# Optimization experiments

Measured on AMD Instinct MI355X. Metric: run time of the kernel, lower is better.

The kernel has to match this reference:

```python
import jax, jax.numpy as jnp
import numpy as np

NUM_HEADS = 16
DIM_MODEL = 1024
DIM_K = DIM_MODEL // NUM_HEADS
B, S = 2, 2048


def _linear_params(key, d_in, d_out):
    kw, kb = jax.random.split(key)
    bound = 1.0 / np.sqrt(d_in)
    W = jax.random.uniform(kw, (d_out, d_in), jnp.float32, -bound, bound)
    b = jax.random.uniform(kb, (d_out,), jnp.float32, -bound, bound)
    return W, b


def setup_inputs() -> dict:
    key = jax.random.key(0)
    ks = jax.random.split(key, 7)
    Q_in = jax.random.normal(ks[0], (B, S, DIM_MODEL), jnp.float32)
    K_in = jax.random.normal(ks[1], (B, S, DIM_MODEL), jnp.float32)
    V_in = jax.random.normal(ks[2], (B, S, DIM_MODEL), jnp.float32)
    Wq, bq = _linear_params(ks[3], DIM_MODEL, DIM_MODEL)
    Wk, bk = _linear_params(ks[4], DIM_MODEL, DIM_MODEL)
    Wv, bv = _linear_params(ks[5], DIM_MODEL, DIM_MODEL)
    Wo, bo = _linear_params(ks[6], DIM_MODEL, DIM_MODEL)
    return {"Q_in": Q_in, "K_in": K_in, "V_in": V_in,
            "Wq": Wq, "bq": bq, "Wk": Wk, "bk": bk,
            "Wv": Wv, "bv": bv, "Wo": Wo, "bo": bo}


def reference(Q_in, K_in, V_in, Wq, bq, Wk, bk, Wv, bv, Wo, bo):
    # QKV projections (nn.Linear: x @ W.T + b)
    Q = Q_in @ Wq.T + bq
    K = K_in @ Wk.T + bk
    V = V_in @ Wv.T + bv
    # [B, S, D] -> [B, H, S, dk]
    def split_heads(x):
        return x.reshape(B, S, NUM_HEADS, DIM_K).transpose(0, 2, 1, 3)
    Qh, Kh, Vh = split_heads(Q), split_heads(K), split_heads(V)
    # Scaled dot-product attention
    scale = 1.0 / np.sqrt(DIM_K)
    scores = jnp.einsum('bhqd,bhkd->bhqk', Qh, Kh) * scale  # [B,H,S,S]
    attn = jax.nn.softmax(scores, axis=-1)
    out = jnp.einsum('bhqk,bhkd->bhqd', attn, Vh)  # [B,H,S,dk]
    # Merge heads -> [B, S, D]
    out = out.transpose(0, 2, 1, 3).reshape(B, S, DIM_MODEL)
    return out @ Wo.T + bo
```

## Files before the change

### kernel.cpp

```cpp
#include <hip/hip_runtime.h>
#include <stdint.h>

#define BB 2
#define SS 2048
#define DD 1024
#define HH 16
#define DKK 64
#define MT (BB*SS)

#define GSTRIDE 40
#define ASTRIDE 72

using short8  = __attribute__((ext_vector_type(8))) short;
using floatx4 = __attribute__((ext_vector_type(4))) float;
using u16x4   = __attribute__((ext_vector_type(4))) unsigned short;
typedef unsigned short u16;

__device__ __forceinline__ u16 f2b(float f) {
  union { float f; unsigned u; } v; v.f = f;
  return (u16)((v.u + 0x7FFFu + ((v.u >> 16) & 1u)) >> 16);
}
__device__ __forceinline__ void pack16(const float4* p, short8& lo, short8& hi) {
  float4 x0 = p[0], x1 = p[1], x2 = p[2], x3 = p[3];
  lo[0]=(short)f2b(x0.x); lo[1]=(short)f2b(x0.y); lo[2]=(short)f2b(x0.z); lo[3]=(short)f2b(x0.w);
  lo[4]=(short)f2b(x1.x); lo[5]=(short)f2b(x1.y); lo[6]=(short)f2b(x1.z); lo[7]=(short)f2b(x1.w);
  hi[0]=(short)f2b(x2.x); hi[1]=(short)f2b(x2.y); hi[2]=(short)f2b(x2.z); hi[3]=(short)f2b(x2.w);
  hi[4]=(short)f2b(x3.x); hi[5]=(short)f2b(x3.y); hi[6]=(short)f2b(x3.z); hi[7]=(short)f2b(x3.w);
}
__device__ __forceinline__ void gload16(const u16* g, u16* l) {
  __builtin_amdgcn_global_load_lds(
      (const __attribute__((address_space(1))) void*)g,
      (__attribute__((address_space(3))) void*)l, 16, 0, 0);
}

__global__ __launch_bounds__(256) void cast_all(
    const float* __restrict__ Qin, const float* __restrict__ Kin,
    const float* __restrict__ Vin, const float* __restrict__ Wq,
    const float* __restrict__ Wk,  const float* __restrict__ Wv,
    const float* __restrict__ Wo,
    u16* __restrict__ cQ, u16* __restrict__ cK, u16* __restrict__ cV,
    u16* __restrict__ cWq, u16* __restrict__ cWk, u16* __restrict__ cWv,
    u16* __restrict__ cWo)
{
  const int y = blockIdx.y;
  if (y >= 3 && blockIdx.x >= (DD*DD/8/256)) return;
  const float* s; u16* d;
  switch (y) {
    case 0: s = Qin; d = cQ;  break;
    case 1: s = Kin; d = cK;  break;
    case 2: s = Vin; d = cV;  break;
    case 3: s = Wq;  d = cWq; break;
    case 4: s = Wk;  d = cWk; break;
    case 5: s = Wv;  d = cWv; break;
    default: s = Wo; d = cWo; break;
  }
  const size_t g = (size_t)blockIdx.x * 256 + threadIdx.x;
  float4 x0 = ((const float4*)s)[g*2], x1 = ((const float4*)s)[g*2+1];
  short8 lo;
  lo[0]=(short)f2b(x0.x); lo[1]=(short)f2b(x0.y); lo[2]=(short)f2b(x0.z); lo[3]=(short)f2b(x0.w);
  lo[4]=(short)f2b(x1.x); lo[5]=(short)f2b(x1.y); lo[6]=(short)f2b(x1.z); lo[7]=(short)f2b(x1.w);
  ((short8*)d)[g] = lo;
}
__global__ __launch_bounds__(256) void cast_w3(
    const float* __restrict__ w0, const float* __restrict__ w1,
    const float* __restrict__ w2, u16* __restrict__ o)
{
  const float* s = (blockIdx.y == 0) ? w0 : (blockIdx.y == 1) ? w1 : w2;
  u16* d = o + (size_t)blockIdx.y * (DD * DD);
  const size_t g = (size_t)blockIdx.x * 256 + threadIdx.x;
  float4 x0 = ((const float4*)s)[g*2], x1 = ((const float4*)s)[g*2+1];
  short8 lo;
  lo[0]=(short)f2b(x0.x); lo[1]=(short)f2b(x0.y); lo[2]=(short)f2b(x0.z); lo[3]=(short)f2b(x0.w);
  lo[4]=(short)f2b(x1.x); lo[5]=(short)f2b(x1.y); lo[6]=(short)f2b(x1.z); lo[7]=(short)f2b(x1.w);
  ((short8*)d)[g] = lo;
}

template<bool OUT_F32>
__device__ __forceinline__ void gemm_async(
    const u16* __restrict__ A, const u16* __restrict__ W,
    const float* __restrict__ bias, void* __restrict__ Cv,
    const int K, const int N, const int m0, const int n0, const float scale)
{
  __shared__ __align__(16) u16 sA[128*64];
  __shared__ __align__(16) u16 sB[128*64];

  const int tid  = threadIdx.x;
  const int wave = tid >> 6;
  const int lane = tid & 63;
  const int quad = lane >> 4;
  const int lr   = lane & 15;
  const int wm   = wave >> 1;
  const int wn   = wave & 1;
  const int srow = lane >> 3;
  const int swz  = (((lane & 7) ^ ((srow & 1) << 2)) << 3);

  floatx4 acc[4][4];
#pragma unroll
  for (int i = 0; i < 4; ++i)
#pragma unroll
    for (int j = 0; j < 4; ++j) acc[i][j] = (floatx4){0.f, 0.f, 0.f, 0.f};

  const u16* pA[4]; const u16* pW[4];
#pragma unroll
  for (int c = 0; c < 4; ++c) {
    const int row = (wave + c*4) * 8 + srow;
    pA[c] = A + (size_t)(m0 + row) * K + swz;
    pW[c] = W + (size_t)(n0 + row) * K + swz;
  }

  const int nk = K >> 6;
  for (int kt = 0; kt < nk; ++kt) {
    const int k0 = kt << 6;
#pragma unroll
    for (int c = 0; c < 4; ++c) {
      gload16(pA[c] + k0, sA + (wave + c*4) * 512);
      gload16(pW[c] + k0, sB + (wave + c*4) * 512);
    }
    __syncthreads();

#pragma unroll
    for (int h2 = 0; h2 < 2; ++h2) {
      const int csel = (quad << 3) + ((h2 ^ (lr & 1)) << 5);
      short8 af[4], bf[4];
#pragma unroll
      for (int t = 0; t < 4; ++t) {
        af[t] = *(const short8*)(sA + (wm*64 + t*16 + lr)*64 + csel);
        bf[t] = *(const short8*)(sB + (wn*64 + t*16 + lr)*64 + csel);
      }
#pragma unroll
      for (int i = 0; i < 4; ++i)
#pragma unroll
        for (int j = 0; j < 4; ++j)
          acc[i][j] = __builtin_amdgcn_mfma_f32_16x16x32_bf16(af[i], bf[j], acc[i][j], 0, 0, 0);
    }
    __syncthreads();
  }

#pragma unroll
  for (int i = 0; i < 4; ++i) {
    const int mb = m0 + wm*64 + i*16 + quad*4;
#pragma unroll
    for (int j = 0; j < 4; ++j) {
      const int n = n0 + wn*64 + j*16 + lr;
      const float bsv = bias[n];
#pragma unroll
      for (int r = 0; r < 4; ++r) {
        const size_t idx = (size_t)(mb + r) * N + n;
        const float v = (acc[i][j][r] + bsv) * scale;
        if (OUT_F32) ((float*)Cv)[idx] = v;
        else         ((u16*)Cv)[idx]   = f2b(v);
      }
    }
  }
}

__global__ __launch_bounds__(256, 3) void gemm_qkv_async(
    const u16* __restrict__ cQ, const u16* __restrict__ cK, const u16* __restrict__ cV,
    const u16* __restrict__ cWq, const u16* __restrict__ cWk, const u16* __restrict__ cWv,
    const float* __restrict__ bq, const float* __restrict__ bk, const float* __restrict__ bv,
    u16* __restrict__ oQ, u16* __restrict__ oK, u16* __restrict__ oV)
{
  const int wsel = blockIdx.x >> 3;
  const int n0 = (blockIdx.x & 7) * 128;
  const int m0 = blockIdx.y * 128;
  const u16* A; const u16* W; const float* bias; u16* C;
  if (wsel == 0)      { A = cQ; W = cWq; bias = bq; C = oQ; }
  else if (wsel == 1) { A = cK; W = cWk; bias = bk; C = oK; }
  else                { A = cV; W = cWv; bias = bv; C = oV; }
  const float scale = (wsel == 0) ? 0.125f : 1.0f;
  gemm_async<false>(A, W, bias, C, DD, DD, m0, n0, scale);
}

__global__ __launch_bounds__(256, 3) void gemm_out_async(
    const u16* __restrict__ A, const u16* __restrict__ cWo,
    const float* __restrict__ bias, float* __restrict__ C)
{
  gemm_async<true>(A, cWo, bias, C, DD, DD, blockIdx.y * 128, blockIdx.x * 128, 1.0f);
}

template<bool A_BF16, bool W_BF16, bool OUT_F32>
__device__ __forceinline__ void gemm_core(
    const void* __restrict__ A, const void* __restrict__ W,
    const float* __restrict__ bias, void* __restrict__ Cv,
    const int K, const int N, const int m0, const int n0, const float scale)
{
  __shared__ __align__(16) u16 sA[128*GSTRIDE];
  __shared__ __align__(16) u16 sB[128*GSTRIDE];

  const int tid  = threadIdx.x;
  const int wave = tid >> 6;
  const int lane = tid & 63;
  const int quad = lane >> 4;
  const int lr   = lane & 15;
  const int wm   = wave >> 1;
  const int wn   = wave & 1;
  const int srow = tid >> 1;
  const int scol = (tid & 1) * 16;

  floatx4 acc[4][4];
#pragma unroll
  for (int i = 0; i < 4; ++i)
#pragma unroll
    for (int j = 0; j < 4; ++j) acc[i][j] = (floatx4){0.f, 0.f, 0.f, 0.f};

  const size_t offA = (size_t)(m0 + srow) * K + scol;
  const size_t offW = (size_t)(n0 + srow) * K + scol;

  const int nk = K >> 5;
  for (int kt = 0; kt < nk; ++kt) {
    const int k0 = kt << 5;
    short8 a0, a1, b0, b1;
    if (A_BF16) {
      const u16* p = (const u16*)A + offA + k0;
      a0 = *(const short8*)p; a1 = *(const short8*)(p + 8);
    } else {
      pack16((const float4*)((const float*)A + offA + k0), a0, a1);
    }
    if (W_BF16) {
      const u16* p = (const u16*)W + offW + k0;
      b0 = *(const short8*)p; b1 = *(const short8*)(p + 8);
    } else {
      pack16((const float4*)((const float*)W + offW + k0), b0, b1);
    }
    __syncthreads();
    *(short8*)(sA + srow * GSTRIDE + scol)     = a0;
    *(short8*)(sA + srow * GSTRIDE + scol + 8) = a1;
    *(short8*)(sB + srow * GSTRIDE + scol)     = b0;
    *(short8*)(sB + srow * GSTRIDE + scol + 8) = b1;
    __syncthreads();

    short8 af[4], bf[4];
#pragma unroll
    for (int t = 0; t < 4; ++t) {
      af[t] = *(const short8*)(sA + (wm*64 + t*16 + lr)*GSTRIDE + quad*8);
      bf[t] = *(const short8*)(sB + (wn*64 + t*16 + lr)*GSTRIDE + quad*8);
    }
#pragma unroll
    for (int i = 0; i < 4; ++i)
#pragma unroll
      for (int j = 0; j < 4; ++j)
        acc[i][j] = __builtin_amdgcn_mfma_f32_16x16x32_bf16(af[i], bf[j], acc[i][j], 0, 0, 0);
  }

#pragma unroll
  for (int i = 0; i < 4; ++i) {
    const int mb = m0 + wm*64 + i*16 + quad*4;
#pragma unroll
    for (int j = 0; j < 4; ++j) {
      const int n = n0 + wn*64 + j*16 + lr;
      const float bsv = bias[n];
#pragma unroll
      for (int r = 0; r < 4; ++r) {
        const size_t idx = (size_t)(mb + r) * N + n;
        const float v = (acc[i][j][r] + bsv) * scale;
        if (OUT_F32) ((float*)Cv)[idx] = v;
        else         ((u16*)Cv)[idx]   = f2b(v);
      }
    }
  }
}

__global__ __launch_bounds__(256, 2) void gemm_qkv_fb(
    const float* __restrict__ Qin, const float* __restrict__ Kin, const float* __restrict__ Vin,
    const u16* __restrict__ cWq, const u16* __restrict__ cWk, const u16* __restrict__ cWv,
    const float* __restrict__ bq, const float* __restrict__ bk, const float* __restrict__ bv,
    u16* __restrict__ oQ, u16* __restrict__ oK, u16* __restrict__ oV)
{
  const int wsel = blockIdx.x >> 3;
  const int n0 = (blockIdx.x & 7) * 128;
  const int m0 = blockIdx.y * 128;
  const float* A; const u16* W; const float* bias; u16* C;
  if (wsel == 0)      { A = Qin; W = cWq; bias = bq; C = oQ; }
  else if (wsel == 1) { A = Kin; W = cWk; bias = bk; C = oK; }
  else                { A = Vin; W = cWv; bias = bv; C = oV; }
  const float scale = (wsel == 0) ? 0.125f : 1.0f;
  gemm_core<false, true, false>(A, W, bias, C, DD, DD, m0, n0, scale);
}
__global__ __launch_bounds__(256, 2) void gemm_out_fb(
    const u16* __restrict__ A, const float* __restrict__ W,
    const float* __restrict__ bias, float* __restrict__ C)
{
  gemm_core<true, false, true>((const void*)A, (const void*)W, bias, C, DD, DD,
                               blockIdx.y * 128, blockIdx.x * 128, 1.0f);
}

__global__ __launch_bounds__(256) void transpose_v(
    const u16* __restrict__ Vp, u16* __restrict__ Vt)
{
  __shared__ u16 t[64 * 65];
  const int st = blockIdx.x, h = blockIdx.y, b = blockIdx.z;

  const int r  = threadIdx.x >> 2;
  const int c0 = (threadIdx.x & 3) * 16;
  const u16* src = Vp + ((size_t)(b * SS + st * 64 + r)) * DD + h * 64 + c0;
  short8 v0 = *(const short8*)src;
  short8 v1 = *(const short8*)(src + 8);
#pragma unroll
  for (int i = 0; i < 8; ++i) {
    t[r * 65 + c0 + i]     = (u16)v0[i];
    t[r * 65 + c0 + 8 + i] = (u16)v1[i];
  }
  __syncthreads();
  union { u16 a[16]; short8 v[2]; } ob;
#pragma unroll
  for (int i = 0; i < 16; ++i) ob.a[i] = t[(c0 + i) * 65 + r];
  u16* dst = Vt + (((size_t)(b * HH + h)) * DKK + r) * SS + st * 64 + c0;
  *(short8*)dst       = ob.v[0];
  *(short8*)(dst + 8) = ob.v[1];
}

__global__ __launch_bounds__(256, 4) void attn(
    const u16* __restrict__ Qp, const u16* __restrict__ Kp,
    const u16* __restrict__ Vt, u16* __restrict__ O)
{
  __shared__ __align__(16) u16 sK[64 * ASTRIDE];
  __shared__ __align__(16) u16 sV[64 * ASTRIDE];
  __shared__ __align__(16) u16 sP[4][32 * ASTRIDE];

  const int tid = threadIdx.x, wave = tid >> 6, lane = tid & 63;
  const int quad = lane >> 4, lr = lane & 15;

  const int flat = (blockIdx.z * 16 + blockIdx.y) * 16 + blockIdx.x;
  const int swzb = (flat & 7) * 64 + (flat >> 3);
  const int qb = swzb & 15;
  const int h  = (swzb >> 4) & 15;
  const int b  = swzb >> 8;
  const size_t vbase = ((size_t)(b * HH + h)) * DKK * SS;

  short8 qf[2][2];
  {
    const u16* qbase = Qp + ((size_t)(b * SS + qb * 128)) * DD + h * 64;
#pragma unroll
    for (int g = 0; g < 2; ++g) {
      const u16* qr = qbase + (size_t)(g*64 + wave*16 + lr) * DD + quad * 8;
      qf[g][0] = *(const short8*)qr;
      qf[g][1] = *(const short8*)(qr + 32);
    }
  }

  floatx4 accO[2][4];
  float m_l[2] = { -3e38f, -3e38f }, l_l[2] = { 0.f, 0.f };
#pragma unroll
  for (int g = 0; g < 2; ++g)
#pragma unroll
    for (int t = 0; t < 4; ++t) accO[g][t] = (floatx4){0.f, 0.f, 0.f, 0.f};

  for (int kt = 0; kt < SS / 64; ++kt) {
    __syncthreads();
    {
      const int r = tid >> 2, c = (tid & 3) * 16;
      const short8* sk = (const short8*)(Kp + ((size_t)(b * SS + kt * 64 + r)) * DD + h * 64 + c);
      short8* dk = (short8*)(sK + r * ASTRIDE + c);
      dk[0] = sk[0]; dk[1] = sk[1];
      const short8* sv = (const short8*)(Vt + vbase + (size_t)r * SS + kt * 64 + c);
      short8* dv = (short8*)(sV + r * ASTRIDE + c);
      dv[0] = sv[0]; dv[1] = sv[1];
    }
    __syncthreads();

#pragma unroll
    for (int g = 0; g < 2; ++g) {
      floatx4 st[4];
#pragma unroll
      for (int t = 0; t < 4; ++t) {
        short8 ka0 = *(const short8*)(sK + (t*16 + lr) * ASTRIDE + quad * 8);
        short8 ka1 = *(const short8*)(sK + (t*16 + lr) * ASTRIDE + 32 + quad * 8);
        floatx4 cc = (floatx4){0.f, 0.f, 0.f, 0.f};
        cc = __builtin_amdgcn_mfma_f32_16x16x32_bf16(ka0, qf[g][0], cc, 0, 0, 0);
        cc = __builtin_amdgcn_mfma_f32_16x16x32_bf16(ka1, qf[g][1], cc, 0, 0, 0);
        st[t] = cc;
      }

      float mx = st[0][0];
#pragma unroll
      for (int t = 0; t < 4; ++t)
#pragma unroll
        for (int r = 0; r < 4; ++r) mx = fmaxf(mx, st[t][r]);
      mx = fmaxf(mx, __shfl_xor(mx, 16, 64));
      mx = fmaxf(mx, __shfl_xor(mx, 32, 64));
      const float mn = fmaxf(m_l[g], mx);
      const float al = __expf(m_l[g] - mn);
      m_l[g] = mn;
      float rs = 0.f;
      u16x4 pk[4];
#pragma unroll
      for (int t = 0; t < 4; ++t)
#pragma unroll
        for (int r = 0; r < 4; ++r) {
          const float p = __expf(st[t][r] - mn);
          rs += p;
          pk[t][r] = f2b(p);
        }
      rs += __shfl_xor(rs, 16, 64);
      rs += __shfl_xor(rs, 32, 64);
      l_l[g] = l_l[g] * al + rs;

      float arow[4];
#pragma unroll
      for (int r = 0; r < 4; ++r) arow[r] = __shfl(al, quad * 4 + r, 64);
#pragma unroll
      for (int t = 0; t < 4; ++t) {
        floatx4 o = accO[g][t];
        o[0] *= arow[0]; o[1] *= arow[1]; o[2] *= arow[2]; o[3] *= arow[3];
        accO[g][t] = o;
      }
#pragma unroll
      for (int t = 0; t < 4; ++t)
        *(u16x4*)(sP[wave] + (g*16 + lr) * ASTRIDE + t * 16 + quad * 4) = pk[t];
    }

    short8 p00 = *(const short8*)(sP[wave] + lr * ASTRIDE + quad * 8);
    short8 p01 = *(const short8*)(sP[wave] + lr * ASTRIDE + 32 + quad * 8);
    short8 p10 = *(const short8*)(sP[wave] + (16 + lr) * ASTRIDE + quad * 8);
    short8 p11 = *(const short8*)(sP[wave] + (16 + lr) * ASTRIDE + 32 + quad * 8);
#pragma unroll
    for (int t = 0; t < 4; ++t) {
      short8 v0 = *(const short8*)(sV + (t*16 + lr) * ASTRIDE + quad * 8);
      short8 v1 = *(const short8*)(sV + (t*16 + lr) * ASTRIDE + 32 + quad * 8);
      accO[0][t] = __builtin_amdgcn_mfma_f32_16x16x32_bf16(p00, v0, accO[0][t], 0, 0, 0);
      accO[0][t] = __builtin_amdgcn_mfma_f32_16x16x32_bf16(p01, v1, accO[0][t], 0, 0, 0);
      accO[1][t] = __builtin_amdgcn_mfma_f32_16x16x32_bf16(p10, v0, accO[1][t], 0, 0, 0);
      accO[1][t] = __builtin_amdgcn_mfma_f32_16x16x32_bf16(p11, v1, accO[1][t], 0, 0, 0);
    }
  }

#pragma unroll
  for (int g = 0; g < 2; ++g) {
    float lrow[4];
#pragma unroll
    for (int r = 0; r < 4; ++r) lrow[r] = __shfl(l_l[g], quad * 4 + r, 64);
#pragma unroll
    for (int t = 0; t < 4; ++t)
#pragma unroll
      for (int r = 0; r < 4; ++r) {
        const int s = qb * 128 + g * 64 + wave * 16 + quad * 4 + r;
        const int d = h * 64 + t * 16 + lr;
        O[((size_t)(b * SS + s)) * DD + d] = f2b(accO[g][t][r] / lrow[r]);
      }
  }
}

extern "C" void kernel_launch(void* const* d_in, const int* in_sizes, int n_in,
                              void* d_out, int out_size, void* d_ws, size_t ws_size,
                              hipStream_t stream)
{
  const float* Qin = (const float*)d_in[0];
  const float* Kin = (const float*)d_in[1];
  const float* Vin = (const float*)d_in[2];
  const float* Wq  = (const float*)d_in[3];
  const float* bq  = (const float*)d_in[4];
  const float* Wk  = (const float*)d_in[5];
  const float* bk  = (const float*)d_in[6];
  const float* Wv  = (const float*)d_in[7];
  const float* bv  = (const float*)d_in[8];
  const float* Wo  = (const float*)d_in[9];
  const float* bo  = (const float*)d_in[10];
  float* out = (float*)d_out;

  const size_t TSZ = (size_t)MT * DD;
  const size_t WSZ = (size_t)DD * DD;
  dim3 blk(256);

  u16* cWq = (u16*)d_out;
  u16* cWk = cWq + WSZ;
  u16* cWv = cWk + WSZ;

  u16* pQ   = (u16*)d_ws;
  u16* pK   = pQ  + TSZ;
  u16* pV   = pK  + TSZ;
  u16* wsVt = pV  + TSZ;
  u16* wsO  = wsVt + TSZ;

  if (ws_size >= (8*TSZ + WSZ) * sizeof(u16)) {
    u16* cQ  = wsO + TSZ;
    u16* cK  = cQ  + TSZ;
    u16* cV  = cK  + TSZ;
    u16* cWo = cV  + TSZ;
    cast_all<<<dim3(TSZ/8/256, 7), blk, 0, stream>>>(
        Qin, Kin, Vin, Wq, Wk, Wv, Wo, cQ, cK, cV, cWq, cWk, cWv, cWo);
    gemm_qkv_async<<<dim3(24, MT/128), blk, 0, stream>>>(
        cQ, cK, cV, cWq, cWk, cWv, bq, bk, bv, pQ, pK, pV);
    transpose_v<<<dim3(SS/64, HH, BB), blk, 0, stream>>>(pV, wsVt);
    attn<<<dim3(SS/128, HH, BB), blk, 0, stream>>>(pQ, pK, wsVt, wsO);
    gemm_out_async<<<dim3(DD/128, MT/128), blk, 0, stream>>>(wsO, cWo, bo, out);
  } else {
    cast_w3<<<dim3(WSZ/8/256, 3), blk, 0, stream>>>(Wq, Wk, Wv, cWq);
    gemm_qkv_fb<<<dim3(24, MT/128), blk, 0, stream>>>(
        Qin, Kin, Vin, cWq, cWk, cWv, bq, bk, bv, pQ, pK, pV);
    transpose_v<<<dim3(SS/64, HH, BB), blk, 0, stream>>>(pV, wsVt);
    attn<<<dim3(SS/128, HH, BB), blk, 0, stream>>>(pQ, pK, wsVt, wsO);
    gemm_out_fb<<<dim3(DD/128, MT/128), blk, 0, stream>>>(wsO, Wo, bo, out);
  }
}
```

Measured before the change: 255.3 us.

## Use 8 waves per attention block with 16 query rows each

The attention kernel moves from 256 threads, each wave owning two 16-row query groups, to 512 threads, each wave owning one 16-row group. Per-wave register state (Q fragments, accumulators, softmax stats) is halved, and the K/V tile load is spread across twice as many threads. This is meant to raise wave-level parallelism and latency hiding per block. In exchange, each K/V tile loaded into shared memory is reused by the same 128 query rows but now across more waves, and barrier synchronisation involves more waves.

```diff
diff --git a/kernel.cpp b/kernel.cpp
--- a/kernel.cpp
+++ b/kernel.cpp
@@ -309,13 +309,13 @@
   *(short8*)(dst + 8) = ob.v[1];
 }
 
-__global__ __launch_bounds__(256, 4) void attn(
+__global__ __launch_bounds__(512, 4) void attn(
     const u16* __restrict__ Qp, const u16* __restrict__ Kp,
     const u16* __restrict__ Vt, u16* __restrict__ O)
 {
   __shared__ __align__(16) u16 sK[64 * ASTRIDE];
   __shared__ __align__(16) u16 sV[64 * ASTRIDE];
-  __shared__ __align__(16) u16 sP[4][32 * ASTRIDE];
+  __shared__ __align__(16) u16 sP[8][16 * ASTRIDE];
 
   const int tid = threadIdx.x, wave = tid >> 6, lane = tid & 63;
   const int quad = lane >> 4, lr = lane & 15;
@@ -327,115 +327,100 @@
   const int b  = swzb >> 8;
   const size_t vbase = ((size_t)(b * HH + h)) * DKK * SS;
 
-  short8 qf[2][2];
+  short8 qf0, qf1;
   {
-    const u16* qbase = Qp + ((size_t)(b * SS + qb * 128)) * DD + h * 64;
-#pragma unroll
-    for (int g = 0; g < 2; ++g) {
-      const u16* qr = qbase + (size_t)(g*64 + wave*16 + lr) * DD + quad * 8;
-      qf[g][0] = *(const short8*)qr;
-      qf[g][1] = *(const short8*)(qr + 32);
-    }
-  }
-
-  floatx4 accO[2][4];
-  float m_l[2] = { -3e38f, -3e38f }, l_l[2] = { 0.f, 0.f };
-#pragma unroll
-  for (int g = 0; g < 2; ++g)
-#pragma unroll
-    for (int t = 0; t < 4; ++t) accO[g][t] = (floatx4){0.f, 0.f, 0.f, 0.f};
+    const u16* qr = Qp + ((size_t)(b * SS + qb * 128 + wave * 16 + lr)) * DD + h * 64 + quad * 8;
+    qf0 = *(const short8*)qr;
+    qf1 = *(const short8*)(qr + 32);
+  }
+
+  floatx4 accO[4];
+  float m_l = -3e38f, l_l = 0.f;
+#pragma unroll
+  for (int t = 0; t < 4; ++t) accO[t] = (floatx4){0.f, 0.f, 0.f, 0.f};
+
+  const int sr = tid >> 3, sc = (tid & 7) * 8;
+  const u16* kg = Kp + ((size_t)(b * SS + sr)) * DD + h * 64 + sc;
+  const u16* vg = Vt + vbase + (size_t)sr * SS + sc;
+  u16* dk = sK + sr * ASTRIDE + sc;
+  u16* dv = sV + sr * ASTRIDE + sc;
 
   for (int kt = 0; kt < SS / 64; ++kt) {
     __syncthreads();
-    {
-      const int r = tid >> 2, c = (tid & 3) * 16;
-      const short8* sk = (const short8*)(Kp + ((size_t)(b * SS + kt * 64 + r)) * DD + h * 64 + c);
-      short8* dk = (short8*)(sK + r * ASTRIDE + c);
-      dk[0] = sk[0]; dk[1] = sk[1];
-      const short8* sv = (const short8*)(Vt + vbase + (size_t)r * SS + kt * 64 + c);
-      short8* dv = (short8*)(sV + r * ASTRIDE + c);
-      dv[0] = sv[0]; dv[1] = sv[1];
-    }
-    __syncthreads();
-
-#pragma unroll
-    for (int g = 0; g < 2; ++g) {
-      floatx4 st[4];
-#pragma unroll
-      for (int t = 0; t < 4; ++t) {
-        short8 ka0 = *(const short8*)(sK + (t*16 + lr) * ASTRIDE + quad * 8);
-        short8 ka1 = *(const short8*)(sK + (t*16 + lr) * ASTRIDE + 32 + quad * 8);
-        floatx4 cc = (floatx4){0.f, 0.f, 0.f, 0.f};
-        cc = __builtin_amdgcn_mfma_f32_16x16x32_bf16(ka0, qf[g][0], cc, 0, 0, 0);
-        cc = __builtin_amdgcn_mfma_f32_16x16x32_bf16(ka1, qf[g][1], cc, 0, 0, 0);
-        st[t] = cc;
+    *(short8*)dk = *(const short8*)(kg + (size_t)(kt * 64) * DD);
+    *(short8*)dv = *(const short8*)(vg + kt * 64);
+    __syncthreads();
+
+    floatx4 st[4];
+#pragma unroll
+    for (int t = 0; t < 4; ++t) {
+      short8 ka0 = *(const short8*)(sK + (t*16 + lr) * ASTRIDE + quad * 8);
+      short8 ka1 = *(const short8*)(sK + (t*16 + lr) * ASTRIDE + 32 + quad * 8);
+      floatx4 cc = (floatx4){0.f, 0.f, 0.f, 0.f};
+      cc = __builtin_amdgcn_mfma_f32_16x16x32_bf16(ka0, qf0, cc, 0, 0, 0);
+      cc = __builtin_amdgcn_mfma_f32_16x16x32_bf16(ka1, qf1, cc, 0, 0, 0);
+      st[t] = cc;
+    }
+
+    float mx = st[0][0];
+#pragma unroll
+    for (int t = 0; t < 4; ++t)
+#pragma unroll
+      for (int r = 0; r < 4; ++r) mx = fmaxf(mx, st[t][r]);
+    mx = fmaxf(mx, __shfl_xor(mx, 16, 64));
+    mx = fmaxf(mx, __shfl_xor(mx, 32, 64));
+    const float mn = fmaxf(m_l, mx);
+    const float al = __expf(m_l - mn);
+    m_l = mn;
+    float rs = 0.f;
+    u16x4 pk[4];
+#pragma unroll
+    for (int t = 0; t < 4; ++t)
+#pragma unroll
+      for (int r = 0; r < 4; ++r) {
+        const float p = __expf(st[t][r] - mn);
+        rs += p;
+        pk[t][r] = f2b(p);
       }
-
-      float mx = st[0][0];
-#pragma unroll
-      for (int t = 0; t < 4; ++t)
-#pragma unroll
-        for (int r = 0; r < 4; ++r) mx = fmaxf(mx, st[t][r]);
-      mx = fmaxf(mx, __shfl_xor(mx, 16, 64));
-      mx = fmaxf(mx, __shfl_xor(mx, 32, 64));
-      const float mn = fmaxf(m_l[g], mx);
-      const float al = __expf(m_l[g] - mn);
-      m_l[g] = mn;
-      float rs = 0.f;
-      u16x4 pk[4];
-#pragma unroll
-      for (int t = 0; t < 4; ++t)
-#pragma unroll
-        for (int r = 0; r < 4; ++r) {
-          const float p = __expf(st[t][r] - mn);
-          rs += p;
-          pk[t][r] = f2b(p);
-        }
-      rs += __shfl_xor(rs, 16, 64);
-      rs += __shfl_xor(rs, 32, 64);
-      l_l[g] = l_l[g] * al + rs;
-
-      float arow[4];
-#pragma unroll
-      for (int r = 0; r < 4; ++r) arow[r] = __shfl(al, quad * 4 + r, 64);
-#pragma unroll
-      for (int t = 0; t < 4; ++t) {
-        floatx4 o = accO[g][t];
-        o[0] *= arow[0]; o[1] *= arow[1]; o[2] *= arow[2]; o[3] *= arow[3];
-        accO[g][t] = o;
-      }
-#pragma unroll
-      for (int t = 0; t < 4; ++t)
-        *(u16x4*)(sP[wave] + (g*16 + lr) * ASTRIDE + t * 16 + quad * 4) = pk[t];
-    }
-
-    short8 p00 = *(const short8*)(sP[wave] + lr * ASTRIDE + quad * 8);
-    short8 p01 = *(const short8*)(sP[wave] + lr * ASTRIDE + 32 + quad * 8);
-    short8 p10 = *(const short8*)(sP[wave] + (16 + lr) * ASTRIDE + quad * 8);
-    short8 p11 = *(const short8*)(sP[wave] + (16 + lr) * ASTRIDE + 32 + quad * 8);
+    rs += __shfl_xor(rs, 16, 64);
+    rs += __shfl_xor(rs, 32, 64);
+    l_l = l_l * al + rs;
+
+    float arow[4];
+#pragma unroll
+    for (int r = 0; r < 4; ++r) arow[r] = __shfl(al, quad * 4 + r, 64);
+#pragma unroll
+    for (int t = 0; t < 4; ++t) {
+      floatx4 o = accO[t];
+      o[0] *= arow[0]; o[1] *= arow[1]; o[2] *= arow[2]; o[3] *= arow[3];
+      accO[t] = o;
+    }
+#pragma unroll
+    for (int t = 0; t < 4; ++t)
+      *(u16x4*)(sP[wave] + lr * ASTRIDE + t * 16 + quad * 4) = pk[t];
+
+    short8 p0 = *(const short8*)(sP[wave] + lr * ASTRIDE + quad * 8);
+    short8 p1 = *(const short8*)(sP[wave] + lr * ASTRIDE + 32 + quad * 8);
 #pragma unroll
     for (int t = 0; t < 4; ++t) {
       short8 v0 = *(const short8*)(sV + (t*16 + lr) * ASTRIDE + quad * 8);
       short8 v1 = *(const short8*)(sV + (t*16 + lr) * ASTRIDE + 32 + quad * 8);
-      accO[0][t] = __builtin_amdgcn_mfma_f32_16x16x32_bf16(p00, v0, accO[0][t], 0, 0, 0);
-      accO[0][t] = __builtin_amdgcn_mfma_f32_16x16x32_bf16(p01, v1, accO[0][t], 0, 0, 0);
-      accO[1][t] = __builtin_amdgcn_mfma_f32_16x16x32_bf16(p10, v0, accO[1][t], 0, 0, 0);
-      accO[1][t] = __builtin_amdgcn_mfma_f32_16x16x32_bf16(p11, v1, accO[1][t], 0, 0, 0);
-    }
-  }
-
-#pragma unroll
-  for (int g = 0; g < 2; ++g) {
+      accO[t] = __builtin_amdgcn_mfma_f32_16x16x32_bf16(p0, v0, accO[t], 0, 0, 0);
+      accO[t] = __builtin_amdgcn_mfma_f32_16x16x32_bf16(p1, v1, accO[t], 0, 0, 0);
+    }
+  }
+
+  {
     float lrow[4];
 #pragma unroll
-    for (int r = 0; r < 4; ++r) lrow[r] = __shfl(l_l[g], quad * 4 + r, 64);
+    for (int r = 0; r < 4; ++r) lrow[r] = __shfl(l_l, quad * 4 + r, 64);
 #pragma unroll
     for (int t = 0; t < 4; ++t)
 #pragma unroll
       for (int r = 0; r < 4; ++r) {
-        const int s = qb * 128 + g * 64 + wave * 16 + quad * 4 + r;
+        const int s = qb * 128 + wave * 16 + quad * 4 + r;
         const int d = h * 64 + t * 16 + lr;
-        O[((size_t)(b * SS + s)) * DD + d] = f2b(accO[g][t][r] / lrow[r]);
+        O[((size_t)(b * SS + s)) * DD + d] = f2b(accO[t][r] / lrow[r]);
       }
   }
 }
@@ -481,14 +466,14 @@
     gemm_qkv_async<<<dim3(24, MT/128), blk, 0, stream>>>(
         cQ, cK, cV, cWq, cWk, cWv, bq, bk, bv, pQ, pK, pV);
     transpose_v<<<dim3(SS/64, HH, BB), blk, 0, stream>>>(pV, wsVt);
-    attn<<<dim3(SS/128, HH, BB), blk, 0, stream>>>(pQ, pK, wsVt, wsO);
+    attn<<<dim3(SS/128, HH, BB), dim3(512), 0, stream>>>(pQ, pK, wsVt, wsO);
     gemm_out_async<<<dim3(DD/128, MT/128), blk, 0, stream>>>(wsO, cWo, bo, out);
   } else {
     cast_w3<<<dim3(WSZ/8/256, 3), blk, 0, stream>>>(Wq, Wk, Wv, cWq);
     gemm_qkv_fb<<<dim3(24, MT/128), blk, 0, stream>>>(
         Qin, Kin, Vin, cWq, cWk, cWv, bq, bk, bv, pQ, pK, pV);
     transpose_v<<<dim3(SS/64, HH, BB), blk, 0, stream>>>(pV, wsVt);
-    attn<<<dim3(SS/128, HH, BB), blk, 0, stream>>>(pQ, pK, wsVt, wsO);
+    attn<<<dim3(SS/128, HH, BB), dim3(512), 0, stream>>>(pQ, pK, wsVt, wsO);
     gemm_out_fb<<<dim3(DD/128, MT/128), blk, 0, stream>>>(wsO, Wo, bo, out);
   }
 }
```

Measured after the change: 258.2 us. Within noise of the previous version (+1.1%).

## Double-buffer K/V tiles with register prefetch and XOR-swizzled LDS in attention

Applied to the files above, without the earlier changes.

The attention kernel now double-buffers K and V tiles in LDS. The next tile is prefetched into registers while the current one is computed, leaving one barrier per iteration instead of two. LDS layouts switch from padded strides to an XOR swizzle to avoid bank conflicts. K and V fragments are hoisted into registers once per tile, and the PV MFMAs are interleaved per row-group with s_setprio hints. The cost is more registers and LDS, with launch bounds lowered from 4 to 2 blocks per CU, which reduces occupancy.

```diff
diff --git a/kernel.cpp b/kernel.cpp
--- a/kernel.cpp
+++ b/kernel.cpp
@@ -9,7 +9,6 @@
 #define MT (BB*SS)
 
 #define GSTRIDE 40
-#define ASTRIDE 72
 
 using short8  = __attribute__((ext_vector_type(8))) short;
 using floatx4 = __attribute__((ext_vector_type(4))) float;
@@ -309,13 +308,17 @@
   *(short8*)(dst + 8) = ob.v[1];
 }
 
-__global__ __launch_bounds__(256, 4) void attn(
+__device__ __forceinline__ int aswz(int row, int cb) {
+  return (row << 7) + (cb ^ ((row & 7) << 4));
+}
+
+__global__ __launch_bounds__(256, 2) void attn(
     const u16* __restrict__ Qp, const u16* __restrict__ Kp,
     const u16* __restrict__ Vt, u16* __restrict__ O)
 {
-  __shared__ __align__(16) u16 sK[64 * ASTRIDE];
-  __shared__ __align__(16) u16 sV[64 * ASTRIDE];
-  __shared__ __align__(16) u16 sP[4][32 * ASTRIDE];
+  __shared__ __align__(16) char sK[2][64 * 128];
+  __shared__ __align__(16) char sV[2][64 * 128];
+  __shared__ __align__(16) char sP[4][32 * 128];
 
   const int tid = threadIdx.x, wave = tid >> 6, lane = tid & 63;
   const int quad = lane >> 4, lr = lane & 15;
@@ -328,14 +331,11 @@
   const size_t vbase = ((size_t)(b * HH + h)) * DKK * SS;
 
   short8 qf[2][2];
-  {
-    const u16* qbase = Qp + ((size_t)(b * SS + qb * 128)) * DD + h * 64;
-#pragma unroll
-    for (int g = 0; g < 2; ++g) {
-      const u16* qr = qbase + (size_t)(g*64 + wave*16 + lr) * DD + quad * 8;
-      qf[g][0] = *(const short8*)qr;
-      qf[g][1] = *(const short8*)(qr + 32);
-    }
+#pragma unroll
+  for (int g = 0; g < 2; ++g) {
+    const u16* qr = Qp + ((size_t)(b * SS + qb * 128 + wave * 32 + g * 16 + lr)) * DD + h * 64 + quad * 8;
+    qf[g][0] = *(const short8*)qr;
+    qf[g][1] = *(const short8*)(qr + 32);
   }
 
   floatx4 accO[2][4];
@@ -345,31 +345,59 @@
 #pragma unroll
     for (int t = 0; t < 4; ++t) accO[g][t] = (floatx4){0.f, 0.f, 0.f, 0.f};
 
-  for (int kt = 0; kt < SS / 64; ++kt) {
-    __syncthreads();
-    {
-      const int r = tid >> 2, c = (tid & 3) * 16;
-      const short8* sk = (const short8*)(Kp + ((size_t)(b * SS + kt * 64 + r)) * DD + h * 64 + c);
-      short8* dk = (short8*)(sK + r * ASTRIDE + c);
-      dk[0] = sk[0]; dk[1] = sk[1];
-      const short8* sv = (const short8*)(Vt + vbase + (size_t)r * SS + kt * 64 + c);
-      short8* dv = (short8*)(sV + r * ASTRIDE + c);
-      dv[0] = sv[0]; dv[1] = sv[1];
-    }
-    __syncthreads();
+  const int sr = tid >> 2;
+  const int ce = (tid & 3) * 16;
+  const u16* kp = Kp + ((size_t)(b * SS + sr)) * DD + h * 64 + ce;
+  const u16* vp = Vt + vbase + (size_t)sr * SS + ce;
+  const int dk0 = aswz(sr, ce * 2), dk1 = aswz(sr, ce * 2 + 16);
+
+  short8 rk0 = *(const short8*)kp,        rk1 = *(const short8*)(kp + 8);
+  short8 rv0 = *(const short8*)vp,        rv1 = *(const short8*)(vp + 8);
+  *(short8*)(sK[0] + dk0) = rk0;  *(short8*)(sK[0] + dk1) = rk1;
+  *(short8*)(sV[0] + dk0) = rv0;  *(short8*)(sV[0] + dk1) = rv1;
+  kp += (size_t)64 * DD; vp += 64;
+  rk0 = *(const short8*)kp;  rk1 = *(const short8*)(kp + 8);
+  rv0 = *(const short8*)vp;  rv1 = *(const short8*)(vp + 8);
+  __syncthreads();
+
+  const int nt = SS / 64;
+  for (int kt = 0; kt < nt; ++kt) {
+    const int cur = kt & 1;
+    if (kt < nt - 1) {
+      *(short8*)(sK[cur ^ 1] + dk0) = rk0;  *(short8*)(sK[cur ^ 1] + dk1) = rk1;
+      *(short8*)(sV[cur ^ 1] + dk0) = rv0;  *(short8*)(sV[cur ^ 1] + dk1) = rv1;
+    }
+    if (kt < nt - 2) {
+      kp += (size_t)64 * DD; vp += 64;
+      rk0 = *(const short8*)kp;  rk1 = *(const short8*)(kp + 8);
+      rv0 = *(const short8*)vp;  rv1 = *(const short8*)(vp + 8);
+    }
+    const char* sKc = sK[cur];
+    const char* sVc = sV[cur];
+    char* sPw = sP[wave];
+
+    short8 kf[4][2], vf[4][2];
+#pragma unroll
+    for (int t = 0; t < 4; ++t) {
+      const int row = t * 16 + lr;
+      kf[t][0] = *(const short8*)(sKc + aswz(row, quad * 16));
+      kf[t][1] = *(const short8*)(sKc + aswz(row, 64 + quad * 16));
+      vf[t][0] = *(const short8*)(sVc + aswz(row, quad * 16));
+      vf[t][1] = *(const short8*)(sVc + aswz(row, 64 + quad * 16));
+    }
 
 #pragma unroll
     for (int g = 0; g < 2; ++g) {
       floatx4 st[4];
+      __builtin_amdgcn_s_setprio(1);
 #pragma unroll
       for (int t = 0; t < 4; ++t) {
-        short8 ka0 = *(const short8*)(sK + (t*16 + lr) * ASTRIDE + quad * 8);
-        short8 ka1 = *(const short8*)(sK + (t*16 + lr) * ASTRIDE + 32 + quad * 8);
         floatx4 cc = (floatx4){0.f, 0.f, 0.f, 0.f};
-        cc = __builtin_amdgcn_mfma_f32_16x16x32_bf16(ka0, qf[g][0], cc, 0, 0, 0);
-        cc = __builtin_amdgcn_mfma_f32_16x16x32_bf16(ka1, qf[g][1], cc, 0, 0, 0);
+        cc = __builtin_amdgcn_mfma_f32_16x16x32_bf16(kf[t][0], qf[g][0], cc, 0, 0, 0);
+        cc = __builtin_amdgcn_mfma_f32_16x16x32_bf16(kf[t][1], qf[g][1], cc, 0, 0, 0);
         st[t] = cc;
       }
+      __builtin_amdgcn_s_setprio(0);
 
       float mx = st[0][0];
 #pragma unroll
@@ -406,22 +434,20 @@
       }
 #pragma unroll
       for (int t = 0; t < 4; ++t)
-        *(u16x4*)(sP[wave] + (g*16 + lr) * ASTRIDE + t * 16 + quad * 4) = pk[t];
-    }
-
-    short8 p00 = *(const short8*)(sP[wave] + lr * ASTRIDE + quad * 8);
-    short8 p01 = *(const short8*)(sP[wave] + lr * ASTRIDE + 32 + quad * 8);
-    short8 p10 = *(const short8*)(sP[wave] + (16 + lr) * ASTRIDE + quad * 8);
-    short8 p11 = *(const short8*)(sP[wave] + (16 + lr) * ASTRIDE + 32 + quad * 8);
-#pragma unroll
-    for (int t = 0; t < 4; ++t) {
-      short8 v0 = *(const short8*)(sV + (t*16 + lr) * ASTRIDE + quad * 8);
-      short8 v1 = *(const short8*)(sV + (t*16 + lr) * ASTRIDE + 32 + quad * 8);
-      accO[0][t] = __builtin_amdgcn_mfma_f32_16x16x32_bf16(p00, v0, accO[0][t], 0, 0, 0);
-      accO[0][t] = __builtin_amdgcn_mfma_f32_16x16x32_bf16(p01, v1, accO[0][t], 0, 0, 0);
-      accO[1][t] = __builtin_amdgcn_mfma_f32_16x16x32_bf16(p10, v0, accO[1][t], 0, 0, 0);
-      accO[1][t] = __builtin_amdgcn_mfma_f32_16x16x32_bf16(p11, v1, accO[1][t], 0, 0, 0);
-    }
+        *(u16x4*)(sPw + aswz(g * 16 + lr, t * 32 + quad * 8)) = pk[t];
+
+      short8 p0 = *(const short8*)(sPw + aswz(g * 16 + lr, quad * 16));
+      short8 p1 = *(const short8*)(sPw + aswz(g * 16 + lr, 64 + quad * 16));
+      __builtin_amdgcn_s_setprio(1);
+#pragma unroll
+      for (int t = 0; t < 4; ++t) {
+        accO[g][t] = __builtin_amdgcn_mfma_f32_16x16x32_bf16(p0, vf[t][0], accO[g][t], 0, 0, 0);
+        accO[g][t] = __builtin_amdgcn_mfma_f32_16x16x32_bf16(p1, vf[t][1], accO[g][t], 0, 0, 0);
+      }
+      __builtin_amdgcn_s_setprio(0);
+    }
+
+    __syncthreads();
   }
 
 #pragma unroll
@@ -433,7 +459,7 @@
     for (int t = 0; t < 4; ++t)
 #pragma unroll
       for (int r = 0; r < 4; ++r) {
-        const int s = qb * 128 + g * 64 + wave * 16 + quad * 4 + r;
+        const int s = qb * 128 + wave * 32 + g * 16 + quad * 4 + r;
         const int d = h * 64 + t * 16 + lr;
         O[((size_t)(b * SS + s)) * DD + d] = f2b(accO[g][t][r] / lrow[r]);
       }
```

Result: no change. 251.2 us (-1.6%).
